# Performance work log

Measured on AMD Instinct MI355X. Metric: run time of the kernel, lower is better.

The kernel has to match this reference:

```python
import jax, jax.numpy as jnp
import numpy as np
from jax import lax

POOL_SIZE = 7
MERGE_INTERVAL = 1
NUM_FRAMES = 16_777_216  # 2**24, indices exact in float32
MAX_BEATS = NUM_FRAMES // 8  # fixed upper bound on number of merged-peak sections


def setup_inputs() -> dict:
    key = jax.random.key(0)
    logit = jax.random.normal(key, (1, NUM_FRAMES), dtype=jnp.float32)
    return {"logit": logit}


def reference(logit):
    # logit: (1, N)
    x = logit[0]  # (N,)
    N = x.shape[0]
    pad = POOL_SIZE // 2
    # max_pool1d, stride 1, same padding
    pooled = lax.reduce_window(x, -jnp.inf, lax.max,
                               window_dimensions=(POOL_SIZE,),
                               window_strides=(1,),
                               padding=((pad, pad),))
    # peak: position is a local max within the window AND value > 0
    peak = (x == pooled) & (x > 0)  # (N,) bool

    idx = jnp.arange(N, dtype=jnp.int32)
    # position of the most recent peak at or before each index (-1 if none)
    last_peak = lax.cummax(jnp.where(peak, idx, jnp.int32(-1)))
    # previous peak strictly before each index
    prev_peak = jnp.concatenate([jnp.full((1,), -1, jnp.int32), last_peak[:-1]])
    gap = idx - prev_peak
    # a peak starts a new section if gap to previous peak > merge_interval (first peak always new)
    is_new = peak & ((gap > MERGE_INTERVAL) | (prev_peak < 0))
    # section id per position (valid only at peaks); sections are contiguous 0..S-1
    section = jnp.cumsum(is_new.astype(jnp.int32)) - 1
    # route non-peaks to an overflow bucket
    seg_ids = jnp.where(peak, section, jnp.int32(MAX_BEATS))

    peak_f = peak.astype(jnp.float32)
    sum_peaks = jax.ops.segment_sum(idx.astype(jnp.float32) * peak_f, seg_ids,
                                    num_segments=MAX_BEATS + 1,
                                    indices_are_sorted=True)[:MAX_BEATS]
    count_peaks = jax.ops.segment_sum(peak_f, seg_ids,
                                      num_segments=MAX_BEATS + 1,
                                      indices_are_sorted=True)[:MAX_BEATS]
    # averaged beat positions; unused sections padded with -1 (torch returns a
    # dynamically-sized (1, num_sections) tensor; here first num_sections entries match)
    beats = jnp.where(count_peaks > 0,
                      sum_peaks / jnp.maximum(count_peaks, 1.0),
                      jnp.float32(-1.0))
    return beats[None, :]  # (1, MAX_BEATS)
```

## Files before the change

kernel.cpp:

```cpp
#include <hip/hip_runtime.h>
#include <cstdint>
#include <math.h>

#define N_FRAMES 16777216
#define MAX_BEATS (N_FRAMES / 8)
#define CHUNK 4096
#define NTHREADS 256
#define NCHUNK (N_FRAMES / CHUNK)
#define NBLK (NCHUNK / 4)
#define TOTAL_MASKS ((size_t)NCHUNK * 64)
#define MAXSEC 2064

typedef unsigned long long u64;
typedef unsigned int u32;

__device__ __forceinline__ float max3f(float a, float b, float c) {
  return fmaxf(fmaxf(a, b), c);
}

__global__ __launch_bounds__(NTHREADS) void k_count(const float* __restrict__ x,
                                                    int* __restrict__ counts,
                                                    u64* __restrict__ masks) {
  __shared__ u32 m16[NTHREADS];
  __shared__ u32 s_pm1;
  const int b = blockIdx.x;
  const int t = threadIdx.x;
  const int lane = t & 63;
  const int gbase = b * CHUNK + t * 16;

  float v[23];
  {
    const float4* p = reinterpret_cast<const float4*>(x + gbase);
#pragma unroll
    for (int k = 0; k < 4; ++k) {
      const float4 f = p[k];
      v[4 + 4 * k] = f.x; v[5 + 4 * k] = f.y; v[6 + 4 * k] = f.z; v[7 + 4 * k] = f.w;
    }
  }
  v[0]  = __shfl_up(v[16], 1, 64);
  v[1]  = __shfl_up(v[17], 1, 64);
  v[2]  = __shfl_up(v[18], 1, 64);
  v[3]  = __shfl_up(v[19], 1, 64);
  v[20] = __shfl_down(v[4], 1, 64);
  v[21] = __shfl_down(v[5], 1, 64);
  v[22] = __shfl_down(v[6], 1, 64);
  if (lane == 0) {
    if (gbase >= 4) {
      const float4 f = *reinterpret_cast<const float4*>(x + gbase - 4);
      v[0] = f.x; v[1] = f.y; v[2] = f.z; v[3] = f.w;
    } else { v[0] = v[1] = v[2] = v[3] = -INFINITY; }
  }
  if (lane == 63) {
    if (gbase + 20 <= N_FRAMES) {
      const float4 f = *reinterpret_cast<const float4*>(x + gbase + 16);
      v[20] = f.x; v[21] = f.y; v[22] = f.z;
    } else { v[20] = v[21] = v[22] = -INFINITY; }
  }

  float Lt[21];
#pragma unroll
  for (int i = 0; i < 21; ++i) Lt[i] = max3f(v[i], v[i + 1], v[i + 2]);

  u32 pm = 0;
#pragma unroll
  for (int e = 0; e < 16; ++e) {
    const float c = v[e + 4];
    const float m = fmaxf(Lt[e + 1], Lt[e + 5]);
    if (c > 0.0f && c >= m) pm |= (1u << e);
  }
  m16[t] = pm;
  if (t == 0) {
    const float c = v[3];
    const float m = fmaxf(Lt[0], Lt[4]);
    s_pm1 = (c > 0.0f && c >= m) ? 1u : 0u;
  }
  __syncthreads();

  if (t < 64) {
    const u64 m = (u64)m16[4 * t] | ((u64)m16[4 * t + 1] << 16) |
                  ((u64)m16[4 * t + 2] << 32) | ((u64)m16[4 * t + 3] << 48);
    masks[((size_t)b << 6) + t] = m;
    const u64 carry = (t == 0) ? (u64)s_pm1 : (u64)((m16[4 * t - 1] >> 15) & 1u);
    int cnt = __popcll(m & ~((m << 1) | carry));
#pragma unroll
    for (int off = 32; off; off >>= 1) cnt += __shfl_down(cnt, off, 64);
    if (t == 0) counts[b] = cnt;
  }
}

__global__ __launch_bounds__(NTHREADS) void k_emit(const u64* __restrict__ masks,
                                                   const int* __restrict__ counts,
                                                   float* __restrict__ out) {
  __shared__ float s_out[4][MAXSEC];
  __shared__ int s_wtot[4];
  __shared__ int s_texcl[NTHREADS];
  __shared__ int s_off[4];
  __shared__ int s_total;
  const int t = threadIdx.x, lane = t & 63, wv = t >> 6;

  int s = 0;
  const int cb = t * 16;
#pragma unroll
  for (int e = 0; e < 16; ++e) s += counts[cb + e];
  int incl = s;
#pragma unroll
  for (int off = 1; off < 64; off <<= 1) {
    const int vv = __shfl_up(incl, off, 64);
    if (lane >= off) incl += vv;
  }
  s_texcl[t] = incl - s;
  if (lane == 63) s_wtot[wv] = incl;
  __syncthreads();
  if (t == 0) s_total = s_wtot[0] + s_wtot[1] + s_wtot[2] + s_wtot[3];
  if (t < 4) {
    const int target = blockIdx.x * 4 + t;
    const int j = target >> 4, r = target & 15;
    int wb = 0;
    for (int ww = 0; ww < (j >> 6); ++ww) wb += s_wtot[ww];
    int pfx = wb + s_texcl[j];
    for (int e = 0; e < r; ++e) pfx += counts[j * 16 + e];
    s_off[t] = pfx;
  }
  __syncthreads();

  const int b = blockIdx.x * 4 + wv;
  const size_t mi = ((size_t)b << 6) + lane;
  const u64 m = masks[mi];
  const u32 myb63 = (u32)(m >> 63);
  u32 prevb = __shfl_up(myb63, 1, 64);
  if (lane == 0) prevb = (b == 0) ? 0u : (u32)(masks[mi - 1] >> 63);
  u64 sm = m & ~((m << 1) | (u64)prevb);
  const int cnt = __popcll(sm);

  int incl2 = cnt;
#pragma unroll
  for (int off = 1; off < 64; off <<= 1) {
    const int vv = __shfl_up(incl2, off, 64);
    if (lane >= off) incl2 += vv;
  }
  const int cnt_chunk = __shfl(incl2, 63, 64);
  int sidl = incl2 - cnt;

  if (s_off[wv] < MAX_BEATS) {
    const int gbase = b * CHUNK + lane * 64;
    u64 smw = sm;
    while (smw) {
      const int sb = __builtin_ctzll(smw);
      smw &= smw - 1;
      const int i0 = gbase + sb;
      const u64 above = m >> sb;
      const int len = (~above == 0ull) ? (64 - sb) : __builtin_ctzll(~above);
      int end = i0 + len - 1;
      if (sb + len == 64) {
        size_t idx = mi + 1;
        while (idx < TOTAL_MASKS) {
          const u64 mm = masks[idx];
          if (~mm == 0ull) { end += 64; ++idx; }
          else { end += __builtin_ctzll(~mm); break; }
        }
      }
      s_out[wv][sidl] = (float)(((double)i0 + (double)end) * 0.5);
      ++sidl;
    }
  }
  __syncthreads();

  if (s_off[wv] < MAX_BEATS) {
    const int off0 = s_off[wv];
    for (int i = lane; i < cnt_chunk; i += 64) {
      const int gi = off0 + i;
      if (gi < MAX_BEATS) out[gi] = s_out[wv][i];
    }
  }

  const int lo = blockIdx.x * (MAX_BEATS / NBLK);
  const int hi = lo + (MAX_BEATS / NBLK);
  for (int i = max(lo, s_total) + t; i < hi; i += NTHREADS)
    out[i] = -1.0f;
}

extern "C" void kernel_launch(void* const* d_in, const int* in_sizes, int n_in,
                              void* d_out, int out_size, void* d_ws, size_t ws_size,
                              hipStream_t stream) {
  const float* x = (const float*)d_in[0];
  float* out = (float*)d_out;

  u64* masks = (u64*)d_ws;
  int* counts = (int*)(masks + TOTAL_MASKS);

  k_count<<<NCHUNK, NTHREADS, 0, stream>>>(x, counts, masks);
  k_emit<<<NBLK, NTHREADS, 0, stream>>>(masks, counts, out);
}
```

Measured before the change: 26.72 us.

## Emit sections with one block per chunk over 16-bit masks

```diff
diff --git a/kernel.cpp b/kernel.cpp
--- a/kernel.cpp
+++ b/kernel.cpp
@@ -7,12 +7,13 @@
 #define CHUNK 4096
 #define NTHREADS 256
 #define NCHUNK (N_FRAMES / CHUNK)
-#define NBLK (NCHUNK / 4)
 #define TOTAL_MASKS ((size_t)NCHUNK * 64)
+#define NMASK16 (NCHUNK * 256)
 #define MAXSEC 2064
 
 typedef unsigned long long u64;
 typedef unsigned int u32;
+typedef unsigned short u16;
 
 __device__ __forceinline__ float max3f(float a, float b, float c) {
   return fmaxf(fmaxf(a, b), c);
@@ -88,20 +89,27 @@
   }
 }
 
-__global__ __launch_bounds__(NTHREADS) void k_emit(const u64* __restrict__ masks,
+__global__ __launch_bounds__(NTHREADS) void k_emit(const u16* __restrict__ masks16,
                                                    const int* __restrict__ counts,
                                                    float* __restrict__ out) {
-  __shared__ float s_out[4][MAXSEC];
+  __shared__ float s_out[MAXSEC];
   __shared__ int s_wtot[4];
   __shared__ int s_texcl[NTHREADS];
-  __shared__ int s_off[4];
+  __shared__ int s_wcnt[4];
+  __shared__ int s_chunk_off;
   __shared__ int s_total;
   const int t = threadIdx.x, lane = t & 63, wv = t >> 6;
+  const int b = blockIdx.x;
 
   int s = 0;
-  const int cb = t * 16;
-#pragma unroll
-  for (int e = 0; e < 16; ++e) s += counts[cb + e];
+  {
+    const int4* c4 = reinterpret_cast<const int4*>(counts + t * 16);
+#pragma unroll
+    for (int e = 0; e < 4; ++e) {
+      const int4 q = c4[e];
+      s += q.x + q.y + q.z + q.w;
+    }
+  }
   int incl = s;
 #pragma unroll
   for (int off = 1; off < 64; off <<= 1) {
@@ -111,26 +119,23 @@
   s_texcl[t] = incl - s;
   if (lane == 63) s_wtot[wv] = incl;
   __syncthreads();
-  if (t == 0) s_total = s_wtot[0] + s_wtot[1] + s_wtot[2] + s_wtot[3];
-  if (t < 4) {
-    const int target = blockIdx.x * 4 + t;
-    const int j = target >> 4, r = target & 15;
+  if (t == 0) {
+    s_total = s_wtot[0] + s_wtot[1] + s_wtot[2] + s_wtot[3];
+    const int j = b >> 4, r = b & 15;
     int wb = 0;
     for (int ww = 0; ww < (j >> 6); ++ww) wb += s_wtot[ww];
     int pfx = wb + s_texcl[j];
     for (int e = 0; e < r; ++e) pfx += counts[j * 16 + e];
-    s_off[t] = pfx;
-  }
-  __syncthreads();
-
-  const int b = blockIdx.x * 4 + wv;
-  const size_t mi = ((size_t)b << 6) + lane;
-  const u64 m = masks[mi];
-  const u32 myb63 = (u32)(m >> 63);
-  u32 prevb = __shfl_up(myb63, 1, 64);
-  if (lane == 0) prevb = (b == 0) ? 0u : (u32)(masks[mi - 1] >> 63);
-  u64 sm = m & ~((m << 1) | (u64)prevb);
-  const int cnt = __popcll(sm);
+    s_chunk_off = pfx;
+  }
+  __syncthreads();
+
+  const int gidx = (b << 8) + t;
+  const u32 pm = masks16[gidx];
+  u32 carry = __shfl_up(pm, 1, 64) >> 15;
+  if (lane == 0) carry = (gidx == 0) ? 0u : ((u32)masks16[gidx - 1] >> 15);
+  u32 sm = pm & ~((pm << 1) | carry);
+  const int cnt = __popc(sm);
 
   int incl2 = cnt;
 #pragma unroll
@@ -138,43 +143,46 @@
     const int vv = __shfl_up(incl2, off, 64);
     if (lane >= off) incl2 += vv;
   }
-  const int cnt_chunk = __shfl(incl2, 63, 64);
-  int sidl = incl2 - cnt;
-
-  if (s_off[wv] < MAX_BEATS) {
-    const int gbase = b * CHUNK + lane * 64;
-    u64 smw = sm;
-    while (smw) {
-      const int sb = __builtin_ctzll(smw);
-      smw &= smw - 1;
+  if (lane == 63) s_wcnt[wv] = incl2;
+  __syncthreads();
+  int woff = 0;
+  for (int ww = 0; ww < wv; ++ww) woff += s_wcnt[ww];
+  const int cnt_chunk = s_wcnt[0] + s_wcnt[1] + s_wcnt[2] + s_wcnt[3];
+  int sidl = woff + incl2 - cnt;
+
+  const int off0 = s_chunk_off;
+  if (off0 < MAX_BEATS) {
+    const int gbase = b * CHUNK + t * 16;
+    while (sm) {
+      const int sb = __builtin_ctz(sm);
+      sm &= sm - 1;
       const int i0 = gbase + sb;
-      const u64 above = m >> sb;
-      const int len = (~above == 0ull) ? (64 - sb) : __builtin_ctzll(~above);
+      const u32 above = pm >> sb;
+      const int len = __builtin_ctz(~above);
       int end = i0 + len - 1;
-      if (sb + len == 64) {
-        size_t idx = mi + 1;
-        while (idx < TOTAL_MASKS) {
-          const u64 mm = masks[idx];
-          if (~mm == 0ull) { end += 64; ++idx; }
-          else { end += __builtin_ctzll(~mm); break; }
+      if (sb + len == 16) {
+        int idx = gidx + 1;
+        while (idx < NMASK16) {
+          const u32 mm = masks16[idx];
+          if (mm == 0xFFFFu) { end += 16; ++idx; }
+          else { end += __builtin_ctz(~mm); break; }
         }
       }
-      s_out[wv][sidl] = (float)(((double)i0 + (double)end) * 0.5);
+      s_out[sidl] = (float)(((double)i0 + (double)end) * 0.5);
       ++sidl;
     }
   }
   __syncthreads();
 
-  if (s_off[wv] < MAX_BEATS) {
-    const int off0 = s_off[wv];
-    for (int i = lane; i < cnt_chunk; i += 64) {
+  if (off0 < MAX_BEATS) {
+    for (int i = t; i < cnt_chunk; i += NTHREADS) {
       const int gi = off0 + i;
-      if (gi < MAX_BEATS) out[gi] = s_out[wv][i];
-    }
-  }
-
-  const int lo = blockIdx.x * (MAX_BEATS / NBLK);
-  const int hi = lo + (MAX_BEATS / NBLK);
+      if (gi < MAX_BEATS) out[gi] = s_out[i];
+    }
+  }
+
+  const int lo = b * (MAX_BEATS / NCHUNK);
+  const int hi = lo + (MAX_BEATS / NCHUNK);
   for (int i = max(lo, s_total) + t; i < hi; i += NTHREADS)
     out[i] = -1.0f;
 }
@@ -189,5 +197,5 @@
   int* counts = (int*)(masks + TOTAL_MASKS);
 
   k_count<<<NCHUNK, NTHREADS, 0, stream>>>(x, counts, masks);
-  k_emit<<<NBLK, NTHREADS, 0, stream>>>(masks, counts, out);
-}
+  k_emit<<<NCHUNK, NTHREADS, 0, stream>>>((const u16*)masks, counts, out);
+}
```

Measured after the change: 29.19 us. 9.3% more time.
